# Performance work log

Hardware: AMD Instinct MI355X
Metric: run time of the kernel (lower is better)

The kernel has to match this reference:

```python
import jax, jax.numpy as jnp
import numpy as np

B, CIN, CMID, COUT, H, W = 4, 64, 128, 128, 128, 128
K = 9  # 3x3 taps
EPS = 1e-5


def conv3x3(x, w, b):
    # standard 3x3 conv, stride 1, pad 1, NCHW / OIHW
    y = jax.lax.conv_general_dilated(x, w, (1, 1), ((1, 1), (1, 1)),
                                     dimension_numbers=('NCHW', 'OIHW', 'NCHW'))
    return y + b[None, :, None, None]


def deform_conv3x3(x, offset, w, b):
    # torchvision DeformConv2d semantics (v1, no mask), kernel 3, pad 1, stride 1.
    # offset: [B, 2*K, H, W] with per-tap (dy, dx) pairs.
    Bn, C, Hn, Wn = x.shape
    off = offset.reshape(Bn, K, 2, Hn, Wn)
    off_y, off_x = off[:, :, 0], off[:, :, 1]          # [B,K,H,W]
    ky = (jnp.arange(K) // 3).astype(x.dtype)          # tap row 0..2
    kx = (jnp.arange(K) % 3).astype(x.dtype)           # tap col 0..2
    # sampling positions: p = out_pos - pad + tap + offset
    py = jnp.arange(Hn, dtype=x.dtype)[None, None, :, None] - 1.0 + ky[None, :, None, None] + off_y
    px = jnp.arange(Wn, dtype=x.dtype)[None, None, None, :] - 1.0 + kx[None, :, None, None] + off_x
    y0 = jnp.floor(py); x0 = jnp.floor(px)
    wy1 = py - y0; wx1 = px - x0                       # bilinear fractions
    y0i = y0.astype(jnp.int32); x0i = x0.astype(jnp.int32)
    xf = x.reshape(Bn, C, Hn * Wn)

    def gather(iy, ix):
        valid = ((iy >= 0) & (iy < Hn) & (ix >= 0) & (ix < Wn)).astype(x.dtype)
        idx = jnp.clip(iy, 0, Hn - 1) * Wn + jnp.clip(ix, 0, Wn - 1)  # [B,K,H,W]
        g = jax.vmap(lambda xb, ib: xb[:, ib])(xf, idx)               # [B,C,K,H,W]
        return g, valid

    g00, v00 = gather(y0i, x0i)
    g01, v01 = gather(y0i, x0i + 1)
    g10, v10 = gather(y0i + 1, x0i)
    g11, v11 = gather(y0i + 1, x0i + 1)

    def wmul(g, v, wgt):
        return g * (v * wgt)[:, None]                  # broadcast over channel dim

    sampled = (wmul(g00, v00, (1 - wy1) * (1 - wx1)) +
               wmul(g01, v01, (1 - wy1) * wx1) +
               wmul(g10, v10, wy1 * (1 - wx1)) +
               wmul(g11, v11, wy1 * wx1))              # [B,C,K,H,W]
    out = jnp.einsum('bckhw,ock->bohw', sampled, w.reshape(w.shape[0], C, K))
    return out + b[None, :, None, None]


def batchnorm_relu(x, gamma, beta):
    # training-mode BN: batch statistics over (N,H,W), biased variance
    mean = jnp.mean(x, axis=(0, 2, 3), keepdims=True)
    var = jnp.mean(jnp.square(x - mean), axis=(0, 2, 3), keepdims=True)
    y = (x - mean) * jax.lax.rsqrt(var + EPS)
    return jax.nn.relu(y * gamma[None, :, None, None] + beta[None, :, None, None])


def setup_inputs() -> dict:
    key = jax.random.key(0)
    ks = jax.random.split(key, 13)
    s = 0.05  # small weights keep offsets small / sampling mostly in-bounds
    return {
        'x': jax.random.normal(ks[0], (B, CIN, H, W), jnp.float32),
        'w_off1': jax.random.normal(ks[1], (2 * K, CIN, 3, 3), jnp.float32) * s,
        'b_off1': jnp.zeros((2 * K,), jnp.float32),
        'w1': jax.random.normal(ks[2], (CMID, CIN, 3, 3), jnp.float32) * s,
        'b1': jax.random.normal(ks[3], (CMID,), jnp.float32) * s,
        'g1': jnp.ones((CMID,), jnp.float32),
        'be1': jnp.zeros((CMID,), jnp.float32),
        'w_off2': jax.random.normal(ks[4], (2 * K, CMID, 3, 3), jnp.float32) * s,
        'b_off2': jnp.zeros((2 * K,), jnp.float32),
        'w2': jax.random.normal(ks[5], (COUT, CMID, 3, 3), jnp.float32) * s,
        'b2': jax.random.normal(ks[6], (COUT,), jnp.float32) * s,
        'g2': jnp.ones((COUT,), jnp.float32),
        'be2': jnp.zeros((COUT,), jnp.float32),
    }


def reference(x, w_off1, b_off1, w1, b1, g1, be1, w_off2, b_off2, w2, b2, g2, be2):
    offset1 = conv3x3(x, w_off1, b_off1)
    out = deform_conv3x3(x, offset1, w1, b1)
    out = batchnorm_relu(out, g1, be1)
    offset2 = conv3x3(out, w_off2, b_off2)
    out = deform_conv3x3(out, offset2, w2, b2)
    out = batchnorm_relu(out, g2, be2)
    return out
```

## Files before the change

### kernel.cpp

```cpp
#include <hip/hip_runtime.h>
#include <hip/hip_bf16.h>

#define BB 4
#define H_ 128
#define W_ 128
#define HWP 16384
#define KOFF 18

typedef short short8 __attribute__((ext_vector_type(8)));
typedef float floatx4 __attribute__((ext_vector_type(4)));

#define WS_AB   16
#define WS_CVT  288
#define CVT_TOTAL 4447396
#define WS_WF1  4447744
#define WS_WF2  4484608
#define WS_XT   4558336
#define WS_Y1   7835136
#define WS_Y1T  16223744
#define WS_XTL  18320896
#define WS_WFO1 20418048
#define WS_WFO2 20436480
#define WS_PART 21600000
#define WS_Y2   WS_Y1

#define R_X     0
#define R_WOFF1 4194304
#define R_BOFF1 4204672
#define R_W1    4204690
#define R_B1    4278418
#define R_G1    4278546
#define R_BE1   4278674
#define R_WOFF2 4278802
#define R_BOFF2 4299538
#define R_W2    4299556
#define R_B2    4447012
#define R_G2    4447140
#define R_BE2   4447268

struct SrcPtrs { const void* p[13]; };

__device__ inline short f2bf(float f) {
    __hip_bfloat16 h = __float2bfloat16(f);
    return *reinterpret_cast<short*>(&h);
}
__device__ inline float bf2f(unsigned short u) {
    return __uint_as_float(((unsigned int)u) << 16);
}
__device__ inline float bfu_lo(unsigned int u) { return __uint_as_float(u << 16); }
__device__ inline float bfu_hi(unsigned int u) { return __uint_as_float(u & 0xFFFF0000u); }
__device__ inline float rl_f(float v, int i) {
    return __int_as_float(__builtin_amdgcn_readlane(__float_as_int(v), i));
}

__global__ void probe_dtype_k(const unsigned int* __restrict__ g1, int* __restrict__ flag) {
    if (threadIdx.x == 0 && blockIdx.x == 0) {
        flag[0] = ((g1[0] & 0xFFFFu) != 0u) ? 1 : 0;
    }
}

__global__ __launch_bounds__(256) void convert_inputs_k(SrcPtrs sp, float* __restrict__ dst,
                                                        const int* __restrict__ flag, int total) {
    int i = blockIdx.x * 256 + threadIdx.x;
    if (i >= total) return;
    constexpr int prefix[13] = {0, R_WOFF1, R_BOFF1, R_W1, R_B1, R_G1, R_BE1,
                                R_WOFF2, R_BOFF2, R_W2, R_B2, R_G2, R_BE2};
    const void* src = sp.p[0];
    int base = 0;
#pragma unroll
    for (int q = 1; q < 13; ++q) {
        if (i >= prefix[q]) { src = sp.p[q]; base = prefix[q]; }
    }
    int local = i - base;
    float v;
    if (flag[0] != 0) {
        v = bf2f(((const unsigned short*)src)[local]);
    } else {
        v = ((const float*)src)[local];
    }
    dst[i] = v;
}

template <int CIN>
__global__ __launch_bounds__(256) void wf_build_k(const float* __restrict__ w, short* __restrict__ wf) {
    constexpr int KSTEPS = CIN * 9 / 32;
    int idx = blockIdx.x * 256 + threadIdx.x;
    int j    = idx & 7;
    int lane = (idx >> 3) & 63;
    int rem  = idx >> 9;
    int ks   = rem % KSTEPS;
    int ct   = rem / KSTEPS;
    int co = ct * 16 + (lane & 15);
    int k  = ks * 32 + (lane >> 4) * 8 + j;
    int ci = k & (CIN - 1);
    int kk = k / CIN;
    wf[idx] = f2bf(w[(co * CIN + ci) * 9 + kk]);
}

template <int CIN>
__global__ __launch_bounds__(256) void wf_off_build_k(const float* __restrict__ w, short* __restrict__ wf) {
    constexpr int KSTEPS = CIN * 9 / 32;
    int idx = blockIdx.x * 256 + threadIdx.x;
    int j    = idx & 7;
    int lane = (idx >> 3) & 63;
    int rem  = idx >> 9;
    int ks   = rem % KSTEPS;
    int cc   = rem / KSTEPS;
    int sel  = cc >> 1;
    int co = (cc & 1) * 16 + (lane & 15);
    int k  = ks * 32 + (lane >> 4) * 8 + j;
    int ci = k & (CIN - 1);
    int kk = k / CIN;
    float v = (co < KOFF) ? w[(co * CIN + ci) * 9 + kk] : 0.f;
    short hi = f2bf(v);
    wf[idx] = sel ? f2bf(v - bf2f((unsigned short)hi)) : hi;
}

__global__ __launch_bounds__(256) void xt_build_k(const float* __restrict__ x,
                                                  unsigned short* __restrict__ xt,
                                                  unsigned short* __restrict__ xtl) {
    __shared__ __align__(4) short s_t[64 * 66];
    __shared__ __align__(4) short s_tl[64 * 66];
    int bi  = blockIdx.x;
    int hw0 = (bi & 255) * 64;
    int b   = bi >> 8;
    int t   = threadIdx.x;
    int hwp = t & 63;
#pragma unroll
    for (int it = 0; it < 16; ++it) {
        int c = it * 4 + (t >> 6);
        float v = x[((long)(b * 64 + c) << 14) + hw0 + hwp];
        short hi = f2bf(v);
        s_t[hwp * 66 + c]  = hi;
        s_tl[hwp * 66 + c] = f2bf(v - bf2f((unsigned short)hi));
    }
    __syncthreads();
#pragma unroll
    for (int it = 0; it < 8; ++it) {
        int i  = it * 256 + t;
        int c2 = (i & 31) * 2;
        int hw2 = i >> 5;
        long da = ((long)((b << 14) + hw0 + hw2)) * 64 + c2;
        *(int*)&xt[da]  = *(const int*)&s_t[hw2 * 66 + c2];
        *(int*)&xtl[da] = *(const int*)&s_tl[hw2 * 66 + c2];
    }
}

__device__ inline int conv_tpk(int h, int w0, int lane, int wv) {
    int tpk = 0;
    if (lane < 36) {
        int r = wv + 8 * lane;
        int p = r & 31;
        int k = r >> 5;
        int y = h - 1 + k / 3;
        int x = w0 + p - 1 + (k % 3);
        int valid = (y >= 0 && y < H_ && x >= 0 && x < W_) ? 1 : 0;
        int yc = min(max(y, 0), H_ - 1), xc = min(max(x, 0), W_ - 1);
        tpk = (yc * W_ + xc) | (valid << 16);
    }
    return tpk;
}

template <int NJ>
__device__ inline void conv_load64(const unsigned short* __restrict__ xb, unsigned int* ub,
                                   int half, int li, int tpk) {
#pragma unroll
    for (int j = 0; j < NJ; ++j) {
        int pkA = __builtin_amdgcn_readlane(tpk, 2 * j);
        int pkB = __builtin_amdgcn_readlane(tpk, 2 * j + 1);
        int pk = half ? pkB : pkA;
        unsigned int u = *(const unsigned int*)(xb + (pk & 0xFFFF) * 64 + 2 * li);
        ub[j] = (pk >> 16) ? u : 0u;
    }
}
template <int NJ, int PADc>
__device__ inline void conv_store64(short* __restrict__ s_samp, const unsigned int* ub,
                                    int half, int li, int wv) {
#pragma unroll
    for (int j = 0; j < NJ; ++j) {
        int r = wv + 8 * (half ? (2 * j + 1) : (2 * j));
        *(unsigned int*)&s_samp[(r & 31) * PADc + (r >> 5) * 64 + 2 * li] = ub[j];
    }
}
template <int I0, int NJ>
__device__ inline void conv_load128(const unsigned short* __restrict__ xb, unsigned int* ub,
                                    int lane, int tpk) {
#pragma unroll
    for (int j = 0; j < NJ; ++j) {
        int pk = __builtin_amdgcn_readlane(tpk, I0 + j);
        unsigned int u = *(const unsigned int*)(xb + (pk & 0xFFFF) * 128 + 2 * lane);
        ub[j] = (pk >> 16) ? u : 0u;
    }
}
template <int I0, int NJ, int KKB, int PADc>
__device__ inline void conv_store128(short* __restrict__ s_samp, const unsigned int* ub,
                                     int wv, int lane) {
#pragma unroll
    for (int j = 0; j < NJ; ++j) {
        int r = wv + 8 * (I0 + j);
        *(unsigned int*)&s_samp[(r & 31) * PADc + ((r >> 5) - KKB) * 128 + 2 * lane] = ub[j];
    }
}

__device__ inline void build_table2_lds(const float* __restrict__ s_off,
                                        int h, int w0, int lane, int wv,
                                        int& tpk, float& tw0, float& tw1, float& tw2, float& tw3) {
    tpk = 0; tw0 = tw1 = tw2 = tw3 = 0.f;
    if (lane < 36) {
        int r = wv + 8 * lane;
        int p = r & 31;
        int k = r >> 5;
        int wpix = w0 + p;
        float oy = s_off[(2 * k) * 32 + p];
        float ox = s_off[(2 * k + 1) * 32 + p];
        float py = (float)(h - 1 + (k / 3)) + oy;
        float px = (float)(wpix - 1 + (k % 3)) + ox;
        float fy = floorf(py), fx = floorf(px);
        float wy = py - fy, wx = px - fx;
        int y0 = (int)fy, x0 = (int)fx;
        int y1 = y0 + 1, x1 = x0 + 1;
        bool vy0 = (y0 >= 0) && (y0 < H_);
        bool vy1 = (y1 >= 0) && (y1 < H_);
        bool vx0 = (x0 >= 0) && (x0 < W_);
        bool vx1 = (x1 >= 0) && (x1 < W_);
        float wy0 = 1.f - wy, wx0 = 1.f - wx;
        tw0 = (vy0 && vx0) ? wy0 * wx0 : 0.f;
        tw1 = (vy0 && vx1) ? wy0 * wx  : 0.f;
        tw2 = (vy1 && vx0) ? wy  * wx0 : 0.f;
        tw3 = (vy1 && vx1) ? wy  * wx  : 0.f;
        int iy0 = min(max(y0, 0), H_ - 1), iy1 = min(max(y1, 0), H_ - 1);
        int ix0 = min(max(x0, 0), W_ - 1), ix1 = min(max(x1, 0), W_ - 1);
        int dx = ix1 - ix0;
        int dy = iy1 - iy0;
        tpk = (iy0 * W_ + ix0) | (dx << 14) | (dy << 15);
    }
}

template <int NB>
__device__ inline void gather_batch128v2(const unsigned short* __restrict__ xb, short* __restrict__ s_samp,
                                         int i0, int kkbase, int wv, int lane,
                                         int tpk, float tw0, float tw1, float tw2, float tw3) {
    constexpr int PADc = 648;
    uint4 ub[NB];
#pragma unroll
    for (int j = 0; j < NB; ++j) {
        int pk = __builtin_amdgcn_readlane(tpk, i0 + j);
        const unsigned short* b00 = xb + (pk & 0x3FFF) * 128;
        const unsigned short* b01 = b00 + ((pk >> 14) & 1) * 128;
        const unsigned short* b10 = b00 + ((pk >> 15) & 1) * (W_ * 128);
        const unsigned short* b11 = b01 + ((pk >> 15) & 1) * (W_ * 128);
        ub[j].x = *(const unsigned int*)(b00 + 2 * lane);
        ub[j].y = *(const unsigned int*)(b01 + 2 * lane);
        ub[j].z = *(const unsigned int*)(b10 + 2 * lane);
        ub[j].w = *(const unsigned int*)(b11 + 2 * lane);
    }
#pragma unroll
    for (int j = 0; j < NB; ++j) {
        int i = i0 + j;
        int r = wv + 8 * i;
        float w00 = rl_f(tw0, i), w01 = rl_f(tw1, i), w10 = rl_f(tw2, i), w11 = rl_f(tw3, i);
        float vlo = w00 * bfu_lo(ub[j].x) + w01 * bfu_lo(ub[j].y)
                  + w10 * bfu_lo(ub[j].z) + w11 * bfu_lo(ub[j].w);
        float vhi = w00 * bfu_hi(ub[j].x) + w01 * bfu_hi(ub[j].y)
                  + w10 * bfu_hi(ub[j].z) + w11 * bfu_hi(ub[j].w);
        __hip_bfloat162 h2 = __float22bfloat162_rn(make_float2(vlo, vhi));
        *(unsigned int*)&s_samp[(r & 31) * PADc + ((r >> 5) - kkbase) * 128 + 2 * lane] =
            *reinterpret_cast<unsigned int*>(&h2);
    }
}

template <int NBP>
__device__ inline void gather_batch64v2(const unsigned short* __restrict__ xb, short* __restrict__ s_samp,
                                        int i0, int wv, int half, int li,
                                        int tpk, float tw0, float tw1, float tw2, float tw3) {
    constexpr int PADc = 584;
    uint4 ub[NBP];
#pragma unroll
    for (int j = 0; j < NBP; ++j) {
        int iA = i0 + 2 * j, iB = iA + 1;
        int pkA = __builtin_amdgcn_readlane(tpk, iA);
        int pkB = __builtin_amdgcn_readlane(tpk, iB);
        int pk = half ? pkB : pkA;
        const unsigned short* b00 = xb + (pk & 0x3FFF) * 64;
        const unsigned short* b01 = b00 + ((pk >> 14) & 1) * 64;
        const unsigned short* b10 = b00 + ((pk >> 15) & 1) * (W_ * 64);
        const unsigned short* b11 = b01 + ((pk >> 15) & 1) * (W_ * 64);
        ub[j].x = *(const unsigned int*)(b00 + 2 * li);
        ub[j].y = *(const unsigned int*)(b01 + 2 * li);
        ub[j].z = *(const unsigned int*)(b10 + 2 * li);
        ub[j].w = *(const unsigned int*)(b11 + 2 * li);
    }
#pragma unroll
    for (int j = 0; j < NBP; ++j) {
        int iA = i0 + 2 * j, iB = iA + 1;
        float w00 = half ? rl_f(tw0, iB) : rl_f(tw0, iA);
        float w01 = half ? rl_f(tw1, iB) : rl_f(tw1, iA);
        float w10 = half ? rl_f(tw2, iB) : rl_f(tw2, iA);
        float w11 = half ? rl_f(tw3, iB) : rl_f(tw3, iA);
        float vlo = w00 * bfu_lo(ub[j].x) + w01 * bfu_lo(ub[j].y)
                  + w10 * bfu_lo(ub[j].z) + w11 * bfu_lo(ub[j].w);
        float vhi = w00 * bfu_hi(ub[j].x) + w01 * bfu_hi(ub[j].y)
                  + w10 * bfu_hi(ub[j].z) + w11 * bfu_hi(ub[j].w);
        __hip_bfloat162 h2 = __float22bfloat162_rn(make_float2(vlo, vhi));
        int r = wv + 8 * (half ? iB : iA);
        *(unsigned int*)&s_samp[(r & 31) * PADc + (r >> 5) * 64 + 2 * li] =
            *reinterpret_cast<unsigned int*>(&h2);
    }
}

__global__ __launch_bounds__(512, 4) void fused64_k(const unsigned short* __restrict__ xt,
                                                    const unsigned short* __restrict__ xtl,
                                                    const short* __restrict__ wfo,
                                                    const float* __restrict__ boff,
                                                    const short* __restrict__ wf,
                                                    const float* __restrict__ bias,
                                                    float* __restrict__ out) {
    constexpr int KSTEPS = 18;
    constexpr int PADc = 584;
    __shared__ __align__(16) short s_samp[32 * PADc];
    __shared__ float s_red[4 * 256];
    __shared__ float s_off[KOFF * 32];

    int bi = blockIdx.x;
    int w0 = (bi & 3) * 32;
    int h  = (bi >> 2) & 127;
    int b  = bi >> 9;
    int t  = threadIdx.x;
    int lane = t & 63;
    int wv   = t >> 6;

    const unsigned short* xbh = xt  + (long)b * HWP * 64;
    const unsigned short* xbl = xtl + (long)b * HWP * 64;
    int half = lane >> 5, li = lane & 31;
    int p_   = lane & 15;
    int quad = lane >> 4;

    {
        int tpkc = conv_tpk(h, w0, lane, wv);
        int c   = wv & 3;
        int ksl = wv >> 2;
        int ct  = c & 1;
        int pt  = c >> 1;
        int row = pt * 16 + p_;
        floatx4 acc;
#pragma unroll
        for (int r = 0; r < 4; ++r) {
            int co = ct * 16 + quad * 4 + r;
            acc[r] = (ksl == 0 && co < KOFF) ? boff[co] : 0.f;
        }

        {
            unsigned int ubh[18];
            conv_load64<18>(xbh, ubh, half, li, tpkc);
            conv_store64<18, PADc>(s_samp, ubh, half, li, wv);
        }
        __syncthreads();
        unsigned int ubl[18];
        conv_load64<18>(xbl, ubl, half, li, tpkc);
#pragma unroll
        for (int ki = 0; ki < 9; ++ki) {
            int ks = ksl * 9 + ki;
            short8 bfr = *(const short8*)&s_samp[row * PADc + ks * 32 + quad * 8];
            short8 ah  = *(const short8*)&wfo[(((long)ct * KSTEPS + ks) * 64 + lane) * 8];
            short8 al  = *(const short8*)&wfo[(((long)(2 + ct) * KSTEPS + ks) * 64 + lane) * 8];
            acc = __builtin_amdgcn_mfma_f32_16x16x32_bf16(ah, bfr, acc, 0, 0, 0);
            acc = __builtin_amdgcn_mfma_f32_16x16x32_bf16(al, bfr, acc, 0, 0, 0);
        }
        __syncthreads();
        conv_store64<18, PADc>(s_samp, ubl, half, li, wv);
        __syncthreads();
#pragma unroll
        for (int ki = 0; ki < 9; ++ki) {
            int ks = ksl * 9 + ki;
            short8 bfr = *(const short8*)&s_samp[row * PADc + ks * 32 + quad * 8];
            short8 ah  = *(const short8*)&wfo[(((long)ct * KSTEPS + ks) * 64 + lane) * 8];
            acc = __builtin_amdgcn_mfma_f32_16x16x32_bf16(ah, bfr, acc, 0, 0, 0);
        }

        if (ksl == 1) {
#pragma unroll
            for (int r = 0; r < 4; ++r) s_red[c * 256 + (quad * 4 + r) * 16 + p_] = acc[r];
        }
        __syncthreads();
        if (ksl == 0) {
#pragma unroll
            for (int r = 0; r < 4; ++r) {
                int co = ct * 16 + quad * 4 + r;
                if (co < KOFF) {
                    s_off[co * 32 + pt * 16 + p_] = acc[r] + s_red[c * 256 + (quad * 4 + r) * 16 + p_];
                }
            }
        }
        __syncthreads();
    }

    int tpk; float tw0, tw1, tw2, tw3;
    build_table2_lds(s_off, h, w0, lane, wv, tpk, tw0, tw1, tw2, tw3);

    gather_batch64v2<6>(xbh, s_samp,  0, wv, half, li, tpk, tw0, tw1, tw2, tw3);
    gather_batch64v2<6>(xbh, s_samp, 12, wv, half, li, tpk, tw0, tw1, tw2, tw3);
    gather_batch64v2<6>(xbh, s_samp, 24, wv, half, li, tpk, tw0, tw1, tw2, tw3);
    __syncthreads();

    int ct = wv;
    floatx4 acc0, acc1;
#pragma unroll
    for (int r = 0; r < 4; ++r) {
        float bv = bias[ct * 16 + quad * 4 + r];
        acc0[r] = bv;
        acc1[r] = bv;
    }
#pragma unroll 3
    for (int ks = 0; ks < KSTEPS; ++ks) {
        short8 a  = *(const short8*)&wf[(((long)ct * KSTEPS + ks) * 64 + lane) * 8];
        short8 b0 = *(const short8*)&s_samp[p_ * PADc + ks * 32 + quad * 8];
        short8 b1 = *(const short8*)&s_samp[(16 + p_) * PADc + ks * 32 + quad * 8];
        acc0 = __builtin_amdgcn_mfma_f32_16x16x32_bf16(a, b0, acc0, 0, 0, 0);
        acc1 = __builtin_amdgcn_mfma_f32_16x16x32_bf16(a, b1, acc1, 0, 0, 0);
    }

    long ob = ((long)(b * 128) << 14) + (h << 7) + w0 + p_;
#pragma unroll
    for (int r = 0; r < 4; ++r) {
        long cpl = (long)(ct * 16 + quad * 4 + r) << 14;
        out[ob + cpl]      = acc0[r];
        out[ob + 16 + cpl] = acc1[r];
    }
}

__global__ __launch_bounds__(512, 4) void fused128_k(const unsigned short* __restrict__ xt,
                                                     const unsigned short* __restrict__ xtl,
                                                     const short* __restrict__ wfo,
                                                     const float* __restrict__ boff,
                                                     const short* __restrict__ wf,
                                                     const float* __restrict__ bias,
                                                     float* __restrict__ out) {
    constexpr int KSTEPS = 36;
    constexpr int PADc = 648;
    __shared__ __align__(16) short s_samp[32 * PADc];
    __shared__ float s_red[4 * 256];
    __shared__ float s_off[KOFF * 32];

    int bi = blockIdx.x;
    int w0 = (bi & 3) * 32;
    int h  = (bi >> 2) & 127;
    int b  = bi >> 9;
    int t  = threadIdx.x;
    int lane = t & 63;
    int wv   = t >> 6;

    const unsigned short* xbh = xt  + (long)b * HWP * 128;
    const unsigned short* xbl = xtl + (long)b * HWP * 128;
    int p_   = lane & 15;
    int quad = lane >> 4;

    {
        int tpkc = conv_tpk(h, w0, lane, wv);
        int c   = wv & 3;
        int ksl = wv >> 2;
        int ct  = c & 1;
        int pt  = c >> 1;
        int row = pt * 16 + p_;
        floatx4 acc;
#pragma unroll
        for (int r = 0; r < 4; ++r) {
            int co = ct * 16 + quad * 4 + r;
            acc[r] = (ksl == 0 && co < KOFF) ? boff[co] : 0.f;
        }

        unsigned int ubA[16], ubB[20];
        conv_load128<0, 16>(xbh, ubA, lane, tpkc);
        conv_store128<0, 16, 0, PADc>(s_samp, ubA, wv, lane);
        __syncthreads();
        conv_load128<16, 20>(xbh, ubB, lane, tpkc);
#pragma unroll
        for (int ki = 0; ki < 8; ++ki) {
            int ks = ksl * 8 + ki;
            short8 bfr = *(const short8*)&s_samp[row * PADc + ks * 32 + quad * 8];
            short8 ah  = *(const short8*)&wfo[(((long)ct * KSTEPS + ks) * 64 + lane) * 8];
            short8 al  = *(const short8*)&wfo[(((long)(2 + ct) * KSTEPS + ks) * 64 + lane) * 8];
            acc = __builtin_amdgcn_mfma_f32_16x16x32_bf16(ah, bfr, acc, 0, 0, 0);
            acc = __builtin_amdgcn_mfma_f32_16x16x32_bf16(al, bfr, acc, 0, 0, 0);
        }
        __syncthreads();
        conv_store128<16, 20, 4, PADc>(s_samp, ubB, wv, lane);
        __syncthreads();
        conv_load128<0, 16>(xbl, ubA, lane, tpkc);
#pragma unroll
        for (int ki = 0; ki < 10; ++ki) {
            int ks = 16 + ksl * 10 + ki;
            short8 bfr = *(const short8*)&s_samp[row * PADc + (ks - 16) * 32 + quad * 8];
            short8 ah  = *(const short8*)&wfo[(((long)ct * KSTEPS + ks) * 64 + lane) * 8];
            short8 al  = *(const short8*)&wfo[(((long)(2 + ct) * KSTEPS + ks) * 64 + lane) * 8];
            acc = __builtin_amdgcn_mfma_f32_16x16x32_bf16(ah, bfr, acc, 0, 0, 0);
            acc = __builtin_amdgcn_mfma_f32_16x16x32_bf16(al, bfr, acc, 0, 0, 0);
        }
        __syncthreads();
        conv_store128<0, 16, 0, PADc>(s_samp, ubA, wv, lane);
        __syncthreads();
        conv_load128<16, 20>(xbl, ubB, lane, tpkc);
#pragma unroll
        for (int ki = 0; ki < 8; ++ki) {
            int ks = ksl * 8 + ki;
            short8 bfr = *(const short8*)&s_samp[row * PADc + ks * 32 + quad * 8];
            short8 ah  = *(const short8*)&wfo[(((long)ct * KSTEPS + ks) * 64 + lane) * 8];
            acc = __builtin_amdgcn_mfma_f32_16x16x32_bf16(ah, bfr, acc, 0, 0, 0);
        }
        __syncthreads();
        conv_store128<16, 20, 4, PADc>(s_samp, ubB, wv, lane);
        __syncthreads();
#pragma unroll
        for (int ki = 0; ki < 10; ++ki) {
            int ks = 16 + ksl * 10 + ki;
            short8 bfr = *(const short8*)&s_samp[row * PADc + (ks - 16) * 32 + quad * 8];
            short8 ah  = *(const short8*)&wfo[(((long)ct * KSTEPS + ks) * 64 + lane) * 8];
            acc = __builtin_amdgcn_mfma_f32_16x16x32_bf16(ah, bfr, acc, 0, 0, 0);
        }

        if (ksl == 1) {
#pragma unroll
            for (int r = 0; r < 4; ++r) s_red[c * 256 + (quad * 4 + r) * 16 + p_] = acc[r];
        }
        __syncthreads();
        if (ksl == 0) {
#pragma unroll
            for (int r = 0; r < 4; ++r) {
                int co = ct * 16 + quad * 4 + r;
                if (co < KOFF) {
                    s_off[co * 32 + pt * 16 + p_] = acc[r] + s_red[c * 256 + (quad * 4 + r) * 16 + p_];
                }
            }
        }
        __syncthreads();
    }

    int tpk; float tw0, tw1, tw2, tw3;
    build_table2_lds(s_off, h, w0, lane, wv, tpk, tw0, tw1, tw2, tw3);

    int ct = wv;
    floatx4 acc0, acc1;
#pragma unroll
    for (int r = 0; r < 4; ++r) {
        float bv = bias[ct * 16 + quad * 4 + r];
        acc0[r] = bv;
        acc1[r] = bv;
    }

    gather_batch128v2<8>(xbh, s_samp, 0, 0, wv, lane, tpk, tw0, tw1, tw2, tw3);
    gather_batch128v2<8>(xbh, s_samp, 8, 0, wv, lane, tpk, tw0, tw1, tw2, tw3);
    __syncthreads();
#pragma unroll 4
    for (int ks = 0; ks < 16; ++ks) {
        short8 a  = *(const short8*)&wf[(((long)ct * KSTEPS + ks) * 64 + lane) * 8];
        short8 b0 = *(const short8*)&s_samp[p_ * PADc + ks * 32 + quad * 8];
        short8 b1 = *(const short8*)&s_samp[(16 + p_) * PADc + ks * 32 + quad * 8];
        acc0 = __builtin_amdgcn_mfma_f32_16x16x32_bf16(a, b0, acc0, 0, 0, 0);
        acc1 = __builtin_amdgcn_mfma_f32_16x16x32_bf16(a, b1, acc1, 0, 0, 0);
    }
    __syncthreads();

    gather_batch128v2<5>(xbh, s_samp, 16, 4, wv, lane, tpk, tw0, tw1, tw2, tw3);
    gather_batch128v2<5>(xbh, s_samp, 21, 4, wv, lane, tpk, tw0, tw1, tw2, tw3);
    gather_batch128v2<5>(xbh, s_samp, 26, 4, wv, lane, tpk, tw0, tw1, tw2, tw3);
    gather_batch128v2<5>(xbh, s_samp, 31, 4, wv, lane, tpk, tw0, tw1, tw2, tw3);
    __syncthreads();
#pragma unroll 4
    for (int ks = 16; ks < KSTEPS; ++ks) {
        short8 a  = *(const short8*)&wf[(((long)ct * KSTEPS + ks) * 64 + lane) * 8];
        short8 b0 = *(const short8*)&s_samp[p_ * PADc + (ks - 16) * 32 + quad * 8];
        short8 b1 = *(const short8*)&s_samp[(16 + p_) * PADc + (ks - 16) * 32 + quad * 8];
        acc0 = __builtin_amdgcn_mfma_f32_16x16x32_bf16(a, b0, acc0, 0, 0, 0);
        acc1 = __builtin_amdgcn_mfma_f32_16x16x32_bf16(a, b1, acc1, 0, 0, 0);
    }

    long ob = ((long)(b * 128) << 14) + (h << 7) + w0 + p_;
#pragma unroll
    for (int r = 0; r < 4; ++r) {
        long cpl = (long)(ct * 16 + quad * 4 + r) << 14;
        out[ob + cpl]      = acc0[r];
        out[ob + 16 + cpl] = acc1[r];
    }
}

__global__ __launch_bounds__(256) void bn_stats_part_k(const float* __restrict__ y, float* __restrict__ part) {
    int bi = blockIdx.x;
    int c = bi & 127;
    int b = bi >> 7;
    int t = threadIdx.x;
    const float4* p4 = (const float4*)(y + ((long)(b * 128 + c) << 14));
    float sum = 0.f, ss = 0.f;
#pragma unroll
    for (int i = 0; i < 16; ++i) {
        float4 v = p4[t + 256 * i];
        sum += v.x + v.y + v.z + v.w;
        ss  += v.x * v.x + v.y * v.y + v.z * v.z + v.w * v.w;
    }
#pragma unroll
    for (int o = 32; o > 0; o >>= 1) { sum += __shfl_down(sum, o); ss += __shfl_down(ss, o); }
    __shared__ float s1[4], s2[4];
    int wave = t >> 6;
    if ((t & 63) == 0) { s1[wave] = sum; s2[wave] = ss; }
    __syncthreads();
    if (t == 0) {
        part[bi]       = s1[0] + s1[1] + s1[2] + s1[3];
        part[512 + bi] = s2[0] + s2[1] + s2[2] + s2[3];
    }
}

__global__ __launch_bounds__(256) void bn_apply_dual_k(const float* __restrict__ y, const float* __restrict__ part,
                                                       const float* __restrict__ g, const float* __restrict__ be,
                                                       unsigned short* __restrict__ yt,
                                                       unsigned short* __restrict__ ytl) {
    __shared__ __align__(4) short s_t[64 * 134];
    __shared__ __align__(4) short s_tl[64 * 134];
    __shared__ float s_a[128], s_sh[128];
    int t = threadIdx.x;
    if (t < 128) {
        float sum = part[t] + part[128 + t] + part[256 + t] + part[384 + t];
        float ss  = part[512 + t] + part[640 + t] + part[768 + t] + part[896 + t];
        float mean = sum * (1.f / 65536.f);
        float var  = ss  * (1.f / 65536.f) - mean * mean;
        float inv  = rsqrtf(var + 1e-5f);
        float a = g[t] * inv;
        s_a[t]  = a;
        s_sh[t] = be[t] - mean * a;
    }
    __syncthreads();

    int bi  = blockIdx.x;
    int hw0 = (bi & 255) * 64;
    int b   = bi >> 8;
    int hwp = t & 63;
#pragma unroll 4
    for (int it = 0; it < 32; ++it) {
        int c = it * 4 + (t >> 6);
        float a = s_a[c], sh = s_sh[c];
        long addr = ((long)(b * 128 + c) << 14) + hw0 + hwp;
        float v = y[addr];
        v = fmaxf(v * a + sh, 0.f);
        short hi = f2bf(v);
        s_t[hwp * 134 + c]  = hi;
        s_tl[hwp * 134 + c] = f2bf(v - bf2f((unsigned short)hi));
    }
    __syncthreads();
#pragma unroll 4
    for (int it = 0; it < 16; ++it) {
        int i   = it * 256 + t;
        int c2  = (i & 63) * 2;
        int hw2 = i >> 6;
        long da = ((long)((b << 14) + hw0 + hw2)) * 128 + c2;
        *(int*)&yt[da]  = *(const int*)&s_t[hw2 * 134 + c2];
        *(int*)&ytl[da] = *(const int*)&s_tl[hw2 * 134 + c2];
    }
}

__global__ __launch_bounds__(256) void bn_apply_out_k(const float* __restrict__ y, const float* __restrict__ part,
                                                      const float* __restrict__ g, const float* __restrict__ be,
                                                      const int* __restrict__ flag, void* __restrict__ out, int total4) {
    __shared__ float s_a[128], s_sh[128];
    int t = threadIdx.x;
    if (t < 128) {
        float sum = part[t] + part[128 + t] + part[256 + t] + part[384 + t];
        float ss  = part[512 + t] + part[640 + t] + part[768 + t] + part[896 + t];
        float mean = sum * (1.f / 65536.f);
        float var  = ss  * (1.f / 65536.f) - mean * mean;
        float inv  = rsqrtf(var + 1e-5f);
        float a = g[t] * inv;
        s_a[t]  = a;
        s_sh[t] = be[t] - mean * a;
    }
    __syncthreads();

    int i = blockIdx.x * 256 + t;
    if (i >= total4) return;
    int c = (i >> 12) & 127;
    float a = s_a[c], sh = s_sh[c];
    float4 v = reinterpret_cast<const float4*>(y)[i];
    v.x = fmaxf(v.x * a + sh, 0.f);
    v.y = fmaxf(v.y * a + sh, 0.f);
    v.z = fmaxf(v.z * a + sh, 0.f);
    v.w = fmaxf(v.w * a + sh, 0.f);
    if (flag[0] != 0) {
        ushort4 u;
        u.x = (unsigned short)f2bf(v.x);
        u.y = (unsigned short)f2bf(v.y);
        u.z = (unsigned short)f2bf(v.z);
        u.w = (unsigned short)f2bf(v.w);
        reinterpret_cast<ushort4*>(out)[i] = u;
    } else {
        reinterpret_cast<float4*>(out)[i] = v;
    }
}

extern "C" void kernel_launch(void* const* d_in, const int* in_sizes, int n_in,
                              void* d_out, int out_size, void* d_ws, size_t ws_size,
                              hipStream_t stream) {
    float* ws   = (float*)d_ws;
    int*   flag = (int*)d_ws;
    float* cvt  = ws + WS_CVT;

    const float* X     = cvt + R_X;
    const float* Woff1 = cvt + R_WOFF1;
    const float* Boff1 = cvt + R_BOFF1;
    const float* W1f   = cvt + R_W1;
    const float* B1f   = cvt + R_B1;
    const float* G1    = cvt + R_G1;
    const float* Be1   = cvt + R_BE1;
    const float* Woff2 = cvt + R_WOFF2;
    const float* Boff2 = cvt + R_BOFF2;
    const float* W2f   = cvt + R_W2;
    const float* B2f   = cvt + R_B2;
    const float* G2    = cvt + R_G2;
    const float* Be2   = cvt + R_BE2;

    short* WF1  = (short*)(ws + WS_WF1);
    short* WF2  = (short*)(ws + WS_WF2);
    short* WFO1 = (short*)(ws + WS_WFO1);
    short* WFO2 = (short*)(ws + WS_WFO2);
    unsigned short* XT   = (unsigned short*)(ws + WS_XT);
    unsigned short* XTL  = (unsigned short*)(ws + WS_XTL);
    unsigned short* Y1T  = (unsigned short*)(ws + WS_Y1T);
    unsigned short* Y1TL = (unsigned short*)(ws + WS_CVT);
    float* PART = ws + WS_PART;
    float* Y1   = ws + WS_Y1;
    float* Y2   = ws + WS_Y2;

    SrcPtrs sp;
    for (int j = 0; j < 13; ++j) sp.p[j] = d_in[j];

    probe_dtype_k<<<1, 64, 0, stream>>>((const unsigned int*)d_in[5], flag);
    convert_inputs_k<<<(CVT_TOTAL + 255) / 256, 256, 0, stream>>>(sp, cvt, flag, CVT_TOTAL);
    wf_build_k<64><<<288, 256, 0, stream>>>(W1f, WF1);
    wf_build_k<128><<<576, 256, 0, stream>>>(W2f, WF2);
    wf_off_build_k<64><<<144, 256, 0, stream>>>(Woff1, WFO1);
    wf_off_build_k<128><<<288, 256, 0, stream>>>(Woff2, WFO2);
    xt_build_k<<<1024, 256, 0, stream>>>(X, XT, XTL);

    fused64_k<<<BB * 128 * 4, 512, 0, stream>>>(XT, XTL, WFO1, Boff1, WF1, B1f, Y1);
    bn_stats_part_k<<<512, 256, 0, stream>>>(Y1, PART);
    bn_apply_dual_k<<<1024, 256, 0, stream>>>(Y1, PART, G1, Be1, Y1T, Y1TL);

    fused128_k<<<BB * 128 * 4, 512, 0, stream>>>(Y1T, Y1TL, WFO2, Boff2, WF2, B2f, Y2);
    bn_stats_part_k<<<512, 256, 0, stream>>>(Y2, PART);
    bn_apply_out_k<<<(BB * 128 * HWP / 4 + 255) / 256, 256, 0, stream>>>(Y2, PART, G2, Be2, flag, d_out, BB * 128 * HWP / 4);
}
```

Baseline: 331.0 us.

## Repartition offset-conv MFMA work so each wave reuses weights across two pixel tiles

In the fused offset-conv prologue of both kernels, warps are remapped from a (channel-tile, pixel-tile, K-half) split to a (channel-tile, K-quarter) split, with each warp covering both 16-pixel tiles. Each weight fragment loaded from global memory now feeds two MFMAs, which halves the weight fragment loads per warp. The cost is a 4-way instead of 2-way K reduction through LDS. The separate s_red buffer is dropped and the reduction reuses the sample buffer, with an extra barrier added, which lowers LDS usage. In the 64-channel kernel the staged gather is also re-split into 16+2 chunks to fit the new K partition, adding more syncs.

```diff
diff --git a/kernel.cpp b/kernel.cpp
--- a/kernel.cpp
+++ b/kernel.cpp
@@ -163,11 +163,12 @@
 
 template <int NJ>
 __device__ inline void conv_load64(const unsigned short* __restrict__ xb, unsigned int* ub,
-                                   int half, int li, int tpk) {
+                                   int half, int li, int tpk, int J0) {
 #pragma unroll
     for (int j = 0; j < NJ; ++j) {
-        int pkA = __builtin_amdgcn_readlane(tpk, 2 * j);
-        int pkB = __builtin_amdgcn_readlane(tpk, 2 * j + 1);
+        int jj = J0 + j;
+        int pkA = __builtin_amdgcn_readlane(tpk, 2 * jj);
+        int pkB = __builtin_amdgcn_readlane(tpk, 2 * jj + 1);
         int pk = half ? pkB : pkA;
         unsigned int u = *(const unsigned int*)(xb + (pk & 0xFFFF) * 64 + 2 * li);
         ub[j] = (pk >> 16) ? u : 0u;
@@ -175,10 +176,11 @@
 }
 template <int NJ, int PADc>
 __device__ inline void conv_store64(short* __restrict__ s_samp, const unsigned int* ub,
-                                    int half, int li, int wv) {
+                                    int half, int li, int wv, int J0) {
 #pragma unroll
     for (int j = 0; j < NJ; ++j) {
-        int r = wv + 8 * (half ? (2 * j + 1) : (2 * j));
+        int jj = J0 + j;
+        int r = wv + 8 * (half ? (2 * jj + 1) : (2 * jj));
         *(unsigned int*)&s_samp[(r & 31) * PADc + (r >> 5) * 64 + 2 * li] = ub[j];
     }
 }
@@ -318,8 +320,8 @@
     constexpr int KSTEPS = 18;
     constexpr int PADc = 584;
     __shared__ __align__(16) short s_samp[32 * PADc];
-    __shared__ float s_red[4 * 256];
     __shared__ float s_off[KOFF * 32];
+    float* s_redf = (float*)s_samp;
 
     int bi = blockIdx.x;
     int w0 = (bi & 3) * 32;
@@ -337,49 +339,85 @@
 
     {
         int tpkc = conv_tpk(h, w0, lane, wv);
-        int c   = wv & 3;
-        int ksl = wv >> 2;
-        int ct  = c & 1;
-        int pt  = c >> 1;
-        int row = pt * 16 + p_;
-        floatx4 acc;
+        int ct  = wv & 1;
+        int ksl = wv >> 1;
+        floatx4 acc0, acc1;
 #pragma unroll
         for (int r = 0; r < 4; ++r) {
             int co = ct * 16 + quad * 4 + r;
-            acc[r] = (ksl == 0 && co < KOFF) ? boff[co] : 0.f;
+            float bv = (ksl == 0 && co < KOFF) ? boff[co] : 0.f;
+            acc0[r] = bv;
+            acc1[r] = bv;
         }
 
         {
-            unsigned int ubh[18];
-            conv_load64<18>(xbh, ubh, half, li, tpkc);
-            conv_store64<18, PADc>(s_samp, ubh, half, li, wv);
-        }
-        __syncthreads();
-        unsigned int ubl[18];
-        conv_load64<18>(xbl, ubl, half, li, tpkc);
-#pragma unroll
-        for (int ki = 0; ki < 9; ++ki) {
-            int ks = ksl * 9 + ki;
-            short8 bfr = *(const short8*)&s_samp[row * PADc + ks * 32 + quad * 8];
-            short8 ah  = *(const short8*)&wfo[(((long)ct * KSTEPS + ks) * 64 + lane) * 8];
-            short8 al  = *(const short8*)&wfo[(((long)(2 + ct) * KSTEPS + ks) * 64 + lane) * 8];
-            acc = __builtin_amdgcn_mfma_f32_16x16x32_bf16(ah, bfr, acc, 0, 0, 0);
-            acc = __builtin_amdgcn_mfma_f32_16x16x32_bf16(al, bfr, acc, 0, 0, 0);
-        }
-        __syncthreads();
-        conv_store64<18, PADc>(s_samp, ubl, half, li, wv);
-        __syncthreads();
-#pragma unroll
-        for (int ki = 0; ki < 9; ++ki) {
-            int ks = ksl * 9 + ki;
-            short8 bfr = *(const short8*)&s_samp[row * PADc + ks * 32 + quad * 8];
-            short8 ah  = *(const short8*)&wfo[(((long)ct * KSTEPS + ks) * 64 + lane) * 8];
-            acc = __builtin_amdgcn_mfma_f32_16x16x32_bf16(ah, bfr, acc, 0, 0, 0);
-        }
-
-        if (ksl == 1) {
-#pragma unroll
-            for (int r = 0; r < 4; ++r) s_red[c * 256 + (quad * 4 + r) * 16 + p_] = acc[r];
+            unsigned int ubA[16];
+            conv_load64<16>(xbh, ubA, half, li, tpkc, 0);
+            conv_store64<16, PADc>(s_samp, ubA, half, li, wv, 0);
+        }
+        __syncthreads();
+        unsigned int ubC[2];
+        conv_load64<2>(xbh, ubC, half, li, tpkc, 16);
+#pragma unroll
+        for (int ki = 0; ki < 4; ++ki) {
+            int ks = ksl * 4 + ki;
+            short8 b0 = *(const short8*)&s_samp[p_ * PADc + ks * 32 + quad * 8];
+            short8 b1 = *(const short8*)&s_samp[(16 + p_) * PADc + ks * 32 + quad * 8];
+            short8 ah = *(const short8*)&wfo[(((long)ct * KSTEPS + ks) * 64 + lane) * 8];
+            short8 al = *(const short8*)&wfo[(((long)(2 + ct) * KSTEPS + ks) * 64 + lane) * 8];
+            acc0 = __builtin_amdgcn_mfma_f32_16x16x32_bf16(ah, b0, acc0, 0, 0, 0);
+            acc0 = __builtin_amdgcn_mfma_f32_16x16x32_bf16(al, b0, acc0, 0, 0, 0);
+            acc1 = __builtin_amdgcn_mfma_f32_16x16x32_bf16(ah, b1, acc1, 0, 0, 0);
+            acc1 = __builtin_amdgcn_mfma_f32_16x16x32_bf16(al, b1, acc1, 0, 0, 0);
+        }
+        __syncthreads();
+        conv_store64<2, PADc>(s_samp, ubC, half, li, wv, 16);
+        __syncthreads();
+        unsigned int ubA2[16];
+        conv_load64<16>(xbl, ubA2, half, li, tpkc, 0);
+        if (ksl < 2) {
+            int ks = 16 + ksl;
+            short8 b0 = *(const short8*)&s_samp[p_ * PADc + ks * 32 + quad * 8];
+            short8 b1 = *(const short8*)&s_samp[(16 + p_) * PADc + ks * 32 + quad * 8];
+            short8 ah = *(const short8*)&wfo[(((long)ct * KSTEPS + ks) * 64 + lane) * 8];
+            short8 al = *(const short8*)&wfo[(((long)(2 + ct) * KSTEPS + ks) * 64 + lane) * 8];
+            acc0 = __builtin_amdgcn_mfma_f32_16x16x32_bf16(ah, b0, acc0, 0, 0, 0);
+            acc0 = __builtin_amdgcn_mfma_f32_16x16x32_bf16(al, b0, acc0, 0, 0, 0);
+            acc1 = __builtin_amdgcn_mfma_f32_16x16x32_bf16(ah, b1, acc1, 0, 0, 0);
+            acc1 = __builtin_amdgcn_mfma_f32_16x16x32_bf16(al, b1, acc1, 0, 0, 0);
+        }
+        __syncthreads();
+        conv_store64<16, PADc>(s_samp, ubA2, half, li, wv, 0);
+        __syncthreads();
+        conv_load64<2>(xbl, ubC, half, li, tpkc, 16);
+#pragma unroll
+        for (int ki = 0; ki < 4; ++ki) {
+            int ks = ksl * 4 + ki;
+            short8 b0 = *(const short8*)&s_samp[p_ * PADc + ks * 32 + quad * 8];
+            short8 b1 = *(const short8*)&s_samp[(16 + p_) * PADc + ks * 32 + quad * 8];
+            short8 ah = *(const short8*)&wfo[(((long)ct * KSTEPS + ks) * 64 + lane) * 8];
+            acc0 = __builtin_amdgcn_mfma_f32_16x16x32_bf16(ah, b0, acc0, 0, 0, 0);
+            acc1 = __builtin_amdgcn_mfma_f32_16x16x32_bf16(ah, b1, acc1, 0, 0, 0);
+        }
+        __syncthreads();
+        conv_store64<2, PADc>(s_samp, ubC, half, li, wv, 16);
+        __syncthreads();
+        if (ksl < 2) {
+            int ks = 16 + ksl;
+            short8 b0 = *(const short8*)&s_samp[p_ * PADc + ks * 32 + quad * 8];
+            short8 b1 = *(const short8*)&s_samp[(16 + p_) * PADc + ks * 32 + quad * 8];
+            short8 ah = *(const short8*)&wfo[(((long)ct * KSTEPS + ks) * 64 + lane) * 8];
+            acc0 = __builtin_amdgcn_mfma_f32_16x16x32_bf16(ah, b0, acc0, 0, 0, 0);
+            acc1 = __builtin_amdgcn_mfma_f32_16x16x32_bf16(ah, b1, acc1, 0, 0, 0);
+        }
+
+        __syncthreads();
+        if (ksl != 0) {
+#pragma unroll
+            for (int r = 0; r < 4; ++r) {
+                s_redf[(((ksl - 1) * 4 + ct * 2 + 0) * 256) + (quad * 4 + r) * 16 + p_] = acc0[r];
+                s_redf[(((ksl - 1) * 4 + ct * 2 + 1) * 256) + (quad * 4 + r) * 16 + p_] = acc1[r];
+            }
         }
         __syncthreads();
         if (ksl == 0) {
@@ -387,7 +425,14 @@
             for (int r = 0; r < 4; ++r) {
                 int co = ct * 16 + quad * 4 + r;
                 if (co < KOFF) {
-                    s_off[co * 32 + pt * 16 + p_] = acc[r] + s_red[c * 256 + (quad * 4 + r) * 16 + p_];
+                    float v0 = acc0[r], v1 = acc1[r];
+#pragma unroll
+                    for (int s = 1; s < 4; ++s) {
+                        v0 += s_redf[(((s - 1) * 4 + ct * 2 + 0) * 256) + (quad * 4 + r) * 16 + p_];
+                        v1 += s_redf[(((s - 1) * 4 + ct * 2 + 1) * 256) + (quad * 4 + r) * 16 + p_];
+                    }
+                    s_off[co * 32 + p_]      = v0;
+                    s_off[co * 32 + 16 + p_] = v1;
                 }
             }
         }
@@ -438,8 +483,8 @@
     constexpr int KSTEPS = 36;
     constexpr int PADc = 648;
     __shared__ __align__(16) short s_samp[32 * PADc];
-    __shared__ float s_red[4 * 256];
     __shared__ float s_off[KOFF * 32];
+    float* s_redf = (float*)s_samp;
 
     int bi = blockIdx.x;
     int w0 = (bi & 3) * 32;
@@ -456,16 +501,15 @@
 
     {
         int tpkc = conv_tpk(h, w0, lane, wv);
-        int c   = wv & 3;
-        int ksl = wv >> 2;
-        int ct  = c & 1;
-        int pt  = c >> 1;
-        int row = pt * 16 + p_;
-        floatx4 acc;
+        int ct  = wv & 1;
+        int ksl = wv >> 1;
+        floatx4 acc0, acc1;
 #pragma unroll
         for (int r = 0; r < 4; ++r) {
             int co = ct * 16 + quad * 4 + r;
-            acc[r] = (ksl == 0 && co < KOFF) ? boff[co] : 0.f;
+            float bv = (ksl == 0 && co < KOFF) ? boff[co] : 0.f;
+            acc0[r] = bv;
+            acc1[r] = bv;
         }
 
         unsigned int ubA[16], ubB[20];
@@ -474,52 +518,66 @@
         __syncthreads();
         conv_load128<16, 20>(xbh, ubB, lane, tpkc);
 #pragma unroll
-        for (int ki = 0; ki < 8; ++ki) {
-            int ks = ksl * 8 + ki;
-            short8 bfr = *(const short8*)&s_samp[row * PADc + ks * 32 + quad * 8];
-            short8 ah  = *(const short8*)&wfo[(((long)ct * KSTEPS + ks) * 64 + lane) * 8];
-            short8 al  = *(const short8*)&wfo[(((long)(2 + ct) * KSTEPS + ks) * 64 + lane) * 8];
-            acc = __builtin_amdgcn_mfma_f32_16x16x32_bf16(ah, bfr, acc, 0, 0, 0);
-            acc = __builtin_amdgcn_mfma_f32_16x16x32_bf16(al, bfr, acc, 0, 0, 0);
+        for (int ki = 0; ki < 4; ++ki) {
+            int ks = ksl * 4 + ki;
+            short8 b0 = *(const short8*)&s_samp[p_ * PADc + ks * 32 + quad * 8];
+            short8 b1 = *(const short8*)&s_samp[(16 + p_) * PADc + ks * 32 + quad * 8];
+            short8 ah = *(const short8*)&wfo[(((long)ct * KSTEPS + ks) * 64 + lane) * 8];
+            short8 al = *(const short8*)&wfo[(((long)(2 + ct) * KSTEPS + ks) * 64 + lane) * 8];
+            acc0 = __builtin_amdgcn_mfma_f32_16x16x32_bf16(ah, b0, acc0, 0, 0, 0);
+            acc0 = __builtin_amdgcn_mfma_f32_16x16x32_bf16(al, b0, acc0, 0, 0, 0);
+            acc1 = __builtin_amdgcn_mfma_f32_16x16x32_bf16(ah, b1, acc1, 0, 0, 0);
+            acc1 = __builtin_amdgcn_mfma_f32_16x16x32_bf16(al, b1, acc1, 0, 0, 0);
         }
         __syncthreads();
         conv_store128<16, 20, 4, PADc>(s_samp, ubB, wv, lane);
         __syncthreads();
         conv_load128<0, 16>(xbl, ubA, lane, tpkc);
 #pragma unroll
-        for (int ki = 0; ki < 10; ++ki) {
-            int ks = 16 + ksl * 10 + ki;
-            short8 bfr = *(const short8*)&s_samp[row * PADc + (ks - 16) * 32 + quad * 8];
-            short8 ah  = *(const short8*)&wfo[(((long)ct * KSTEPS + ks) * 64 + lane) * 8];
-            short8 al  = *(const short8*)&wfo[(((long)(2 + ct) * KSTEPS + ks) * 64 + lane) * 8];
-            acc = __builtin_amdgcn_mfma_f32_16x16x32_bf16(ah, bfr, acc, 0, 0, 0);
-            acc = __builtin_amdgcn_mfma_f32_16x16x32_bf16(al, bfr, acc, 0, 0, 0);
+        for (int ki = 0; ki < 5; ++ki) {
+            int ks = 16 + ksl * 5 + ki;
+            short8 b0 = *(const short8*)&s_samp[p_ * PADc + (ks - 16) * 32 + quad * 8];
+            short8 b1 = *(const short8*)&s_samp[(16 + p_) * PADc + (ks - 16) * 32 + quad * 8];
+            short8 ah = *(const short8*)&wfo[(((long)ct * KSTEPS + ks) * 64 + lane) * 8];
+            short8 al = *(const short8*)&wfo[(((long)(2 + ct) * KSTEPS + ks) * 64 + lane) * 8];
+            acc0 = __builtin_amdgcn_mfma_f32_16x16x32_bf16(ah, b0, acc0, 0, 0, 0);
+            acc0 = __builtin_amdgcn_mfma_f32_16x16x32_bf16(al, b0, acc0, 0, 0, 0);
+            acc1 = __builtin_amdgcn_mfma_f32_16x16x32_bf16(ah, b1, acc1, 0, 0, 0);
+            acc1 = __builtin_amdgcn_mfma_f32_16x16x32_bf16(al, b1, acc1, 0, 0, 0);
         }
         __syncthreads();
         conv_store128<0, 16, 0, PADc>(s_samp, ubA, wv, lane);
         __syncthreads();
         conv_load128<16, 20>(xbl, ubB, lane, tpkc);
 #pragma unroll
-        for (int ki = 0; ki < 8; ++ki) {
-            int ks = ksl * 8 + ki;
-            short8 bfr = *(const short8*)&s_samp[row * PADc + ks * 32 + quad * 8];
-            short8 ah  = *(const short8*)&wfo[(((long)ct * KSTEPS + ks) * 64 + lane) * 8];
-            acc = __builtin_amdgcn_mfma_f32_16x16x32_bf16(ah, bfr, acc, 0, 0, 0);
+        for (int ki = 0; ki < 4; ++ki) {
+            int ks = ksl * 4 + ki;
+            short8 b0 = *(const short8*)&s_samp[p_ * PADc + ks * 32 + quad * 8];
+            short8 b1 = *(const short8*)&s_samp[(16 + p_) * PADc + ks * 32 + quad * 8];
+            short8 ah = *(const short8*)&wfo[(((long)ct * KSTEPS + ks) * 64 + lane) * 8];
+            acc0 = __builtin_amdgcn_mfma_f32_16x16x32_bf16(ah, b0, acc0, 0, 0, 0);
+            acc1 = __builtin_amdgcn_mfma_f32_16x16x32_bf16(ah, b1, acc1, 0, 0, 0);
         }
         __syncthreads();
         conv_store128<16, 20, 4, PADc>(s_samp, ubB, wv, lane);
         __syncthreads();
 #pragma unroll
-        for (int ki = 0; ki < 10; ++ki) {
-            int ks = 16 + ksl * 10 + ki;
-            short8 bfr = *(const short8*)&s_samp[row * PADc + (ks - 16) * 32 + quad * 8];
-            short8 ah  = *(const short8*)&wfo[(((long)ct * KSTEPS + ks) * 64 + lane) * 8];
-            acc = __builtin_amdgcn_mfma_f32_16x16x32_bf16(ah, bfr, acc, 0, 0, 0);
-        }
-
-        if (ksl == 1) {
-#pragma unroll
-            for (int r = 0; r < 4; ++r) s_red[c * 256 + (quad * 4 + r) * 16 + p_] = acc[r];
+        for (int ki = 0; ki < 5; ++ki) {
+            int ks = 16 + ksl * 5 + ki;
+            short8 b0 = *(const short8*)&s_samp[p_ * PADc + (ks - 16) * 32 + quad * 8];
+            short8 b1 = *(const short8*)&s_samp[(16 + p_) * PADc + (ks - 16) * 32 + quad * 8];
+            short8 ah = *(const short8*)&wfo[(((long)ct * KSTEPS + ks) * 64 + lane) * 8];
+            acc0 = __builtin_amdgcn_mfma_f32_16x16x32_bf16(ah, b0, acc0, 0, 0, 0);
+            acc1 = __builtin_amdgcn_mfma_f32_16x16x32_bf16(ah, b1, acc1, 0, 0, 0);
+        }
+
+        __syncthreads();
+        if (ksl != 0) {
+#pragma unroll
+            for (int r = 0; r < 4; ++r) {
+                s_redf[(((ksl - 1) * 4 + ct * 2 + 0) * 256) + (quad * 4 + r) * 16 + p_] = acc0[r];
+                s_redf[(((ksl - 1) * 4 + ct * 2 + 1) * 256) + (quad * 4 + r) * 16 + p_] = acc1[r];
+            }
         }
         __syncthreads();
         if (ksl == 0) {
@@ -527,7 +585,14 @@
             for (int r = 0; r < 4; ++r) {
                 int co = ct * 16 + quad * 4 + r;
                 if (co < KOFF) {
-                    s_off[co * 32 + pt * 16 + p_] = acc[r] + s_red[c * 256 + (quad * 4 + r) * 16 + p_];
+                    float v0 = acc0[r], v1 = acc1[r];
+#pragma unroll
+                    for (int s = 1; s < 4; ++s) {
+                        v0 += s_redf[(((s - 1) * 4 + ct * 2 + 0) * 256) + (quad * 4 + r) * 16 + p_];
+                        v1 += s_redf[(((s - 1) * 4 + ct * 2 + 1) * 256) + (quad * 4 + r) * 16 + p_];
+                    }
+                    s_off[co * 32 + p_]      = v0;
+                    s_off[co * 32 + 16 + p_] = v1;
                 }
             }
         }
```

Measured after the change: 297.2 us. 10.2% less time.
